# Optimization experiments

Hardware: AMD Instinct MI355X
Metric: run time of the kernel (lower is better)

The kernel has to match this reference:

```python
import jax, jax.numpy as jnp
import numpy as np

B, NPATCH, PDIM, DIM, OUTD = 4, 1024, 768, 512, 512
DIN, DSTATE, DTRANK, KCONV, NBLK = 2 * DIM, 16, DIM // 16, 4, 2


def _ln(x, w, b, eps=1e-5):
    m = jnp.mean(x, -1, keepdims=True)
    v = jnp.var(x, -1, keepdims=True)
    return (x - m) * jax.lax.rsqrt(v + eps) * w + b


def _mamba_block(x, ln_w, ln_b, in_W, conv_w, conv_b, xproj_W, dt_W, dt_b, A_log, Dp, out_W):
    # x: [b, L, dim]
    b, L, _ = x.shape
    xn = _ln(x, ln_w, ln_b)
    xz = xn @ in_W                                # [b, L, 2*DIN]
    u, z = jnp.split(xz, 2, axis=-1)              # each [b, L, DIN]
    # causal depthwise conv over time
    uc = jnp.transpose(u, (0, 2, 1))              # [b, DIN, L]
    uc = jax.lax.conv_general_dilated(
        uc, conv_w[:, None, :], window_strides=(1,), padding=((KCONV - 1, 0),),
        feature_group_count=DIN)
    uc = uc + conv_b[None, :, None]
    u = jax.nn.silu(jnp.transpose(uc, (0, 2, 1)))  # [b, L, DIN]
    x_dbl = u @ xproj_W                            # [b, L, DTRANK+2*DSTATE]
    dt, Bm, Cm = jnp.split(x_dbl, [DTRANK, DTRANK + DSTATE], axis=-1)
    delta = jax.nn.softplus(dt @ dt_W + dt_b)      # [b, L, DIN]
    A = -jnp.exp(A_log)                            # [DIN, DSTATE]
    dA = jnp.exp(delta[..., None] * A)             # [b, L, DIN, DSTATE]
    dBu = delta[..., None] * Bm[:, :, None, :] * u[..., None]  # [b, L, DIN, DSTATE]
    # selective scan over time
    def step(h, inp):
        dA_t, dBu_t, C_t = inp                     # [b,DIN,DSTATE],[b,DIN,DSTATE],[b,DSTATE]
        h = dA_t * h + dBu_t
        y = jnp.einsum('bdn,bn->bd', h, C_t)
        return h, y
    h0 = jnp.zeros((b, DIN, DSTATE), x.dtype)
    _, ys = jax.lax.scan(step, h0, (jnp.swapaxes(dA, 0, 1), jnp.swapaxes(dBu, 0, 1), jnp.swapaxes(Cm, 0, 1)))
    y = jnp.swapaxes(ys, 0, 1) + u * Dp            # [b, L, DIN]
    y = y * jax.nn.silu(z)
    return x + y @ out_W                           # residual


def setup_inputs() -> dict:
    key = jax.random.key(0)
    ks = iter(jax.random.split(key, 40))
    rn = lambda shape, s=0.02: jax.random.normal(next(ks), shape, jnp.float32) * s
    d = {
        'img': jax.random.normal(next(ks), (B, NPATCH, PDIM), jnp.float32),
        'patch_W': rn((PDIM, DIM)), 'patch_b': jnp.zeros((DIM,), jnp.float32),
        'pos_emb': rn((1, NPATCH + 1, DIM), 1.0), 'cls_tok': rn((1, 1, DIM), 1.0),
        'blk_ln_w': jnp.ones((NBLK, DIM)), 'blk_ln_b': jnp.zeros((NBLK, DIM)),
        'blk_in_W': rn((NBLK, DIM, 2 * DIN)),
        'blk_conv_w': rn((NBLK, DIN, KCONV), 0.1), 'blk_conv_b': jnp.zeros((NBLK, DIN)),
        'blk_xproj_W': rn((NBLK, DIN, DTRANK + 2 * DSTATE)),
        'blk_dt_W': rn((NBLK, DTRANK, DIN), 0.1), 'blk_dt_b': jnp.full((NBLK, DIN), -4.0),
        'blk_A_log': jnp.tile(jnp.log(jnp.arange(1, DSTATE + 1, dtype=jnp.float32))[None, None, :], (NBLK, DIN, 1)),
        'blk_D': jnp.ones((NBLK, DIN)),
        'blk_out_W': rn((NBLK, DIN, DIM)),
        'sl1_W': rn((DIM, OUTD)), 'sl1_b': jnp.zeros((OUTD,)),
        'sl1_lnw': jnp.ones((OUTD,)), 'sl1_lnb': jnp.zeros((OUTD,)),
        'sl2_W': rn((OUTD, OUTD)), 'sl2_b': jnp.zeros((OUTD,)),
        'sl2_lnw': jnp.ones((OUTD,)), 'sl2_lnb': jnp.zeros((OUTD,)),
        'lat_lnw': jnp.ones((OUTD,)), 'lat_lnb': jnp.zeros((OUTD,)),
    }
    return d


def reference(img, patch_W, patch_b, pos_emb, cls_tok,
              blk_ln_w, blk_ln_b, blk_in_W, blk_conv_w, blk_conv_b,
              blk_xproj_W, blk_dt_W, blk_dt_b, blk_A_log, blk_D, blk_out_W,
              sl1_W, sl1_b, sl1_lnw, sl1_lnb, sl2_W, sl2_b, sl2_lnw, sl2_lnb,
              lat_lnw, lat_lnb):
    x = img @ patch_W + patch_b                       # [b, n, dim]
    b, n, _ = x.shape
    cls = jnp.broadcast_to(cls_tok, (b, 1, DIM))
    x = jnp.concatenate([cls, x], axis=1) + pos_emb[:, :n + 1]
    for i in range(NBLK):
        x = _mamba_block(x, blk_ln_w[i], blk_ln_b[i], blk_in_W[i], blk_conv_w[i],
                         blk_conv_b[i], blk_xproj_W[i], blk_dt_W[i], blk_dt_b[i],
                         blk_A_log[i], blk_D[i], blk_out_W[i])
    y = jax.nn.gelu(_ln(x @ sl1_W + sl1_b, sl1_lnw, sl1_lnb), approximate=False)
    a = jax.nn.gelu(_ln(y @ sl2_W + sl2_b, sl2_lnw, sl2_lnb), approximate=False)
    z = jax.nn.softmax(a, axis=1)                     # softmax over sequence dim
    pooled = jnp.sum(y * z, axis=1)                   # [b, outdim]
    return _ln(pooled, lat_lnw, lat_lnb)
```

## Files before the change

### kernel.cpp

```cpp
#include <hip/hip_runtime.h>
#include <cstdint>
#include <cstddef>

#define B_     4
#define NPATCH 1024
#define LSEQ   1025
#define PDIM   768
#define DIM    512
#define OUTD   512
#define DIN    1024
#define DSTATE 16
#define DTRANK 32
#define KCONV  4
#define NBLK   2
#define MROWS  (B_*LSEQ)
#define NSEG_SP 17

typedef unsigned short u16;
typedef __attribute__((ext_vector_type(8))) short bf16x8;
typedef __attribute__((ext_vector_type(4))) float f32x4;

__device__ __forceinline__ float sigmoidf_(float x){ return 1.f/(1.f+__expf(-x)); }
__device__ __forceinline__ float geluf_(float x){ return 0.5f*x*(1.f+erff(x*0.70710678118654752f)); }
__device__ __forceinline__ u16 f2bf(float x){
    uint32_t b = __float_as_uint(x);
    b += 0x7FFFu + ((b >> 16) & 1u);
    return (u16)(b >> 16);
}
__device__ __forceinline__ float bf2f(u16 v){ return __uint_as_float((uint32_t)v << 16); }
template<int CTRL>
__device__ __forceinline__ float dppmov(float x){
    return __int_as_float(__builtin_amdgcn_update_dpp(0, __float_as_int(x), CTRL, 0xF, 0xF, true));
}
__device__ __forceinline__ float red16(float p){
    p += dppmov<0xB1>(p);
    p += dppmov<0x4E>(p);
    p += dppmov<0x141>(p);
    p += dppmov<0x140>(p);
    return p;
}
__device__ __forceinline__ void gload16(const void* g, void* l){
    __builtin_amdgcn_global_load_lds((const __attribute__((address_space(1))) void*)g,
                                     (__attribute__((address_space(3))) void*)l, 16, 0, 0);
}
__device__ __forceinline__ float softplusf_(float v){
    return (v > 20.f) ? v : log1pf(__expf(v));
}

template<int MF>
__global__ __launch_bounds__(256) void gemm_mfma(
    const u16* __restrict__ A, int lda,
    const u16* __restrict__ Wt,
    float* __restrict__ C, int ldc,
    int M, int N, int K,
    const float* __restrict__ bias,
    const float* __restrict__ addsrc,
    int act, u16* __restrict__ bf16out)
{
    __shared__ u16 lsA[MF*32*32];
    __shared__ u16 lsB[128*32];
    const int tid = threadIdx.x;
    const int wid = tid >> 6, lane = tid & 63;
    const int m0 = blockIdx.y * (MF*32), n0 = blockIdx.x * 128;
    const int wm = (wid>>1)*(MF*16), wn = (wid&1)*64;
    f32x4 acc[MF][4] = {};

    const char* Agp = (const char*)(A + (size_t)m0 * lda);
    const char* Bgp = (const char*)(Wt + (size_t)n0 * K);
    const int lrow = lane >> 2;
    const int lcb  = (((lane & 3) ^ ((lane >> 3) & 3))) * 16;
    const int rsw  = ((lane & 15) >> 1) & 3;
    const int acol = ((lane >> 4) ^ rsw) * 8;

    for (int k0 = 0; k0 < K; k0 += 32) {
        {
            int ra = wid*(MF*8) + lrow;
            gload16(Agp + (size_t)ra*(lda*2) + k0*2 + lcb, &lsA[(wid*(MF*8))*32]);
            if constexpr (MF == 4) {
                gload16(Agp + (size_t)(ra+16)*(lda*2) + k0*2 + lcb, &lsA[(wid*(MF*8)+16)*32]);
            }
        }
        {
            int rb = wid*32 + lrow;
            gload16(Bgp + (size_t)rb*(K*2) + k0*2 + lcb, &lsB[(wid*32)*32]);
            gload16(Bgp + (size_t)(rb+16)*(K*2) + k0*2 + lcb, &lsB[(wid*32+16)*32]);
        }
        __syncthreads();
        bf16x8 af[MF], bfr[4];
        #pragma unroll
        for (int i = 0; i < MF; ++i)
            af[i] = *(const bf16x8*)&lsA[(wm + i*16 + (lane&15))*32 + acol];
        #pragma unroll
        for (int j = 0; j < 4; ++j)
            bfr[j] = *(const bf16x8*)&lsB[(wn + j*16 + (lane&15))*32 + acol];
        #pragma unroll
        for (int i = 0; i < MF; ++i)
            #pragma unroll
            for (int j = 0; j < 4; ++j)
                acc[i][j] = __builtin_amdgcn_mfma_f32_16x16x32_bf16(af[i], bfr[j], acc[i][j], 0, 0, 0);
        __syncthreads();
    }
    #pragma unroll
    for (int i = 0; i < MF; ++i) {
        #pragma unroll
        for (int j = 0; j < 4; ++j) {
            int col = n0 + wn + j*16 + (lane & 15);
            float bv = bias ? bias[col] : 0.f;
            #pragma unroll
            for (int r = 0; r < 4; ++r) {
                int row = m0 + wm + i*16 + (lane>>4)*4 + r;
                if (row < M) {
                    float v = acc[i][j][r] + bv;
                    if (addsrc) v += addsrc[(size_t)row*ldc + col];
                    if (act == 1) v = softplusf_(v);
                    if (C) C[(size_t)row*ldc + col] = v;
                    if (bf16out) bf16out[(size_t)row*ldc + col] = f2bf(v);
                }
            }
        }
    }
}

__global__ __launch_bounds__(256) void xproj_gemm(
    const float* __restrict__ Au,
    const float* __restrict__ W,
    float* __restrict__ P)
{
    __shared__ float As[16][68];
    __shared__ float Bs[16][68];
    int tid = threadIdx.x;
    int tx = tid & 15, ty = tid >> 4;
    int m0 = blockIdx.x * 64;
    int kbase = blockIdx.y * 256;
    float acc[4][4] = {};
    for (int k0 = kbase; k0 < kbase + 256; k0 += 16) {
        {
            int r  = tid >> 2;
            int kq = (tid & 3) << 2;
            float4 va = make_float4(0.f,0.f,0.f,0.f);
            int gr = m0 + r;
            if (gr < MROWS) va = *reinterpret_cast<const float4*>(Au + (size_t)gr*DIN + k0 + kq);
            As[kq+0][r]=va.x; As[kq+1][r]=va.y; As[kq+2][r]=va.z; As[kq+3][r]=va.w;
        }
        {
            int kk = tid >> 4;
            int nq = (tid & 15) << 2;
            float4 vb = *reinterpret_cast<const float4*>(W + (size_t)(k0+kk)*64 + nq);
            Bs[kk][nq+0]=vb.x; Bs[kk][nq+1]=vb.y; Bs[kk][nq+2]=vb.z; Bs[kk][nq+3]=vb.w;
        }
        __syncthreads();
        #pragma unroll
        for (int k = 0; k < 16; ++k) {
            float a0=As[k][ty*4+0],a1=As[k][ty*4+1],a2=As[k][ty*4+2],a3=As[k][ty*4+3];
            float b0=Bs[k][tx*4+0],b1=Bs[k][tx*4+1],b2=Bs[k][tx*4+2],b3=Bs[k][tx*4+3];
            acc[0][0]=fmaf(a0,b0,acc[0][0]); acc[0][1]=fmaf(a0,b1,acc[0][1]);
            acc[0][2]=fmaf(a0,b2,acc[0][2]); acc[0][3]=fmaf(a0,b3,acc[0][3]);
            acc[1][0]=fmaf(a1,b0,acc[1][0]); acc[1][1]=fmaf(a1,b1,acc[1][1]);
            acc[1][2]=fmaf(a1,b2,acc[1][2]); acc[1][3]=fmaf(a1,b3,acc[1][3]);
            acc[2][0]=fmaf(a2,b0,acc[2][0]); acc[2][1]=fmaf(a2,b1,acc[2][1]);
            acc[2][2]=fmaf(a2,b2,acc[2][2]); acc[2][3]=fmaf(a2,b3,acc[2][3]);
            acc[3][0]=fmaf(a3,b0,acc[3][0]); acc[3][1]=fmaf(a3,b1,acc[3][1]);
            acc[3][2]=fmaf(a3,b2,acc[3][2]); acc[3][3]=fmaf(a3,b3,acc[3][3]);
        }
        __syncthreads();
    }
    float* Pp = P + (size_t)blockIdx.y * (MROWS*64);
    #pragma unroll
    for (int i = 0; i < 4; ++i) {
        int r = m0 + ty*4 + i;
        if (r >= MROWS) continue;
        #pragma unroll
        for (int j = 0; j < 4; ++j)
            Pp[(size_t)r*64 + tx*4 + j] = acc[i][j];
    }
}

__global__ __launch_bounds__(256) void xproj_reduce(
    const float* __restrict__ P, float* __restrict__ xdbl)
{
    int idx = blockIdx.x*256 + threadIdx.x;
    xdbl[idx] = P[idx] + P[MROWS*64 + idx] + P[2*MROWS*64 + idx] + P[3*MROWS*64 + idx];
}

__device__ void tcast(const float* __restrict__ in, u16* __restrict__ outp,
                      int K, int N, int tix)
{
    __shared__ float tl[32][33];
    int ntn = N >> 5;
    int tk = tix / ntn, tn = tix - tk*ntn;
    int tid = threadIdx.x;
    int r = tid >> 3, c0 = (tid & 7) << 2;
    float4 v = *(const float4*)&in[(size_t)(tk*32 + r)*N + tn*32 + c0];
    tl[r][c0+0]=v.x; tl[r][c0+1]=v.y; tl[r][c0+2]=v.z; tl[r][c0+3]=v.w;
    __syncthreads();
    int nn = r, k0 = c0;
    uint32_t w0 = f2bf(tl[k0+0][nn]) | ((uint32_t)f2bf(tl[k0+1][nn]) << 16);
    uint32_t w1 = f2bf(tl[k0+2][nn]) | ((uint32_t)f2bf(tl[k0+3][nn]) << 16);
    uint2 o; o.x = w0; o.y = w1;
    *(uint2*)&outp[(size_t)(tn*32 + nn)*K + tk*32 + k0] = o;
}

__global__ __launch_bounds__(256) void prep_kernel(
    const float* __restrict__ img, const float* __restrict__ pW,
    const float* __restrict__ inW, const float* __restrict__ outW,
    const float* __restrict__ s1W, const float* __restrict__ s2W,
    u16* imgb, u16* pWt, u16* inWt, u16* outWt, u16* s1t, u16* s2t)
{
    int b = blockIdx.x;
    if (b < 3072) {
        int idx = b*1024 + threadIdx.x*4;
        float4 v = *(const float4*)&img[idx];
        uint2 o;
        o.x = f2bf(v.x) | ((uint32_t)f2bf(v.y) << 16);
        o.y = f2bf(v.z) | ((uint32_t)f2bf(v.w) << 16);
        *(uint2*)&imgb[idx] = o;
        return;
    }
    b -= 3072;
    if (b < 384)  { tcast(pW, pWt, 768, 512, b); return; }
    b -= 384;
    if (b < 2048) { int blk=b>>10, t=b&1023; tcast(inW + (size_t)blk*512*2048, inWt + (size_t)blk*1048576, 512, 2048, t); return; }
    b -= 2048;
    if (b < 1024) { int blk=b>>9, t=b&511; tcast(outW + (size_t)blk*1024*512, outWt + (size_t)blk*524288, 1024, 512, t); return; }
    b -= 1024;
    if (b < 256)  { tcast(s1W, s1t, 512, 512, b); return; }
    b -= 256;
    tcast(s2W, s2t, 512, 512, b);
}

__global__ __launch_bounds__(256) void assemble_x(
    const float* __restrict__ tmp, const float* __restrict__ cls,
    const float* __restrict__ pos, float* __restrict__ x)
{
    int idx = blockIdx.x*256 + threadIdx.x;
    int d = idx & 511;
    int r = idx >> 9;
    int l = r % LSEQ;
    int b = r / LSEQ;
    float v = (l == 0) ? cls[d] : tmp[((size_t)(b*NPATCH + l-1))*DIM + d];
    x[idx] = v + pos[(size_t)l*DIM + d];
}

__global__ __launch_bounds__(256) void ln_act(
    const float* __restrict__ in, const float* __restrict__ gw, const float* __restrict__ gb,
    float* __restrict__ f32out, u16* __restrict__ bf16out, int act)
{
    int row = blockIdx.x;
    const float* p = in + (size_t)row * 512;
    int t = threadIdx.x;
    float v0 = p[t], v1 = p[t + 256];
    float s = v0 + v1, q = v0*v0 + v1*v1;
    #pragma unroll
    for (int o = 32; o; o >>= 1) { s += __shfl_xor(s, o); q += __shfl_xor(q, o); }
    __shared__ float ls[4], lq[4];
    int w = t >> 6;
    if ((t & 63) == 0) { ls[w] = s; lq[w] = q; }
    __syncthreads();
    s = ls[0]+ls[1]+ls[2]+ls[3];
    q = lq[0]+lq[1]+lq[2]+lq[3];
    float mean = s * (1.f/512.f);
    float var  = q * (1.f/512.f) - mean*mean;
    float inv  = rsqrtf(var + 1e-5f);
    float o0 = (v0-mean)*inv*gw[t]     + gb[t];
    float o1 = (v1-mean)*inv*gw[t+256] + gb[t+256];
    if (act == 2) { o0 = geluf_(o0); o1 = geluf_(o1); }
    if (f32out)  { f32out[(size_t)row*512 + t] = o0; f32out[(size_t)row*512 + t + 256] = o1; }
    if (bf16out) { bf16out[(size_t)row*512 + t] = f2bf(o0); bf16out[(size_t)row*512 + t + 256] = f2bf(o1); }
}

__global__ __launch_bounds__(256) void conv_silu(
    const u16* __restrict__ xzb, const float* __restrict__ cw,
    const float* __restrict__ cb, float* __restrict__ uo)
{
    int idx = blockIdx.x*256 + threadIdx.x;
    int dq = idx & 255;
    int r  = idx >> 8;
    int b = r / LSEQ, l = r - b*LSEQ;
    int d0 = dq << 2;
    float4 w0 = *(const float4*)&cw[(d0+0)*4];
    float4 w1 = *(const float4*)&cw[(d0+1)*4];
    float4 w2 = *(const float4*)&cw[(d0+2)*4];
    float4 w3 = *(const float4*)&cw[(d0+3)*4];
    float4 acc = *(const float4*)&cb[d0];
    const float* wv0 = &w0.x; const float* wv1 = &w1.x;
    const float* wv2 = &w2.x; const float* wv3 = &w3.x;
    #pragma unroll
    for (int k = 0; k < KCONV; ++k) {
        int ls = l - (KCONV-1) + k;
        if (ls >= 0) {
            ushort4 v = *(const ushort4*)&xzb[((size_t)(b*LSEQ + ls))*2048 + d0];
            acc.x = fmaf(wv0[k], bf2f(v.x), acc.x);
            acc.y = fmaf(wv1[k], bf2f(v.y), acc.y);
            acc.z = fmaf(wv2[k], bf2f(v.z), acc.z);
            acc.w = fmaf(wv3[k], bf2f(v.w), acc.w);
        }
    }
    acc.x *= sigmoidf_(acc.x);
    acc.y *= sigmoidf_(acc.y);
    acc.z *= sigmoidf_(acc.z);
    acc.w *= sigmoidf_(acc.w);
    *(float4*)&uo[(size_t)r*DIN + d0] = acc;
}

__global__ __launch_bounds__(256) void scan_phase1(
    const float* __restrict__ u,    const float* __restrict__ xdbl,
    const float* __restrict__ dtW,  const float* __restrict__ dtb,
    const float* __restrict__ A_log,
    float* __restrict__ Aseg, float* __restrict__ Hseg)
{
    const int dg = blockIdx.x, b = blockIdx.y, s = blockIdx.z;
    const int tid = threadIdx.x;
    const int n = tid & 15, dl = tid >> 4;
    const int tr = tid >> 4, tc = tid & 15;
    const int d0 = dg*16, d = d0 + dl;
    const float Adn2 = -__expf(A_log[(size_t)d*DSTATE + n]) * 1.44269504f;
    __shared__ float sX[16][68];
    __shared__ float sW[32][17];
    __shared__ float sU[16][20];
    __shared__ float sDel[16][20];
    {
        int k = tid >> 4;
        sW[k][tc]    = dtW[(size_t)k*DIN + d0 + tc];
        sW[k+16][tc] = dtW[(size_t)(k+16)*DIN + d0 + tc];
    }
    const float db = dtb[d0 + tc];
    float sdv = 0.f, h = 0.f;
    const size_t base = (size_t)b*LSEQ + (size_t)s*128;
    for (int c0 = 0; c0 < 128; c0 += 16) {
        __syncthreads();
        {
            size_t row = base + c0 + tr;
            *(float4*)&sX[tr][tc*4] = *(const float4*)&xdbl[row*64 + tc*4];
            sU[tc][tr] = u[row*DIN + d0 + tc];
        }
        __syncthreads();
        {
            float acc = db;
            #pragma unroll
            for (int k = 0; k < 32; ++k) acc = fmaf(sX[tr][k], sW[k][tc], acc);
            sDel[tc][tr] = softplusf_(acc);
        }
        __syncthreads();
        #pragma unroll
        for (int hf = 0; hf < 2; ++hf) {
            f32x4 vD0 = *(const f32x4*)&sDel[dl][hf*8];
            f32x4 vD1 = *(const f32x4*)&sDel[dl][hf*8+4];
            f32x4 vU0 = *(const f32x4*)&sU[dl][hf*8];
            f32x4 vU1 = *(const f32x4*)&sU[dl][hf*8+4];
            #pragma unroll
            for (int t = 0; t < 8; ++t) {
                float dv = (t<4) ? vD0[t&3] : vD1[t&3];
                float uv = (t<4) ? vU0[t&3] : vU1[t&3];
                float Bv = sX[hf*8+t][32+n];
                sdv += dv;
                h = fmaf(__builtin_exp2f(dv * Adn2), h, dv*uv*Bv);
            }
        }
    }
    int dn = d*DSTATE + n;
    Aseg[((size_t)b*7 + s)*16384 + dn] = __builtin_exp2f(Adn2 * sdv);
    Hseg[((size_t)b*8 + s)*16384 + dn] = h;
}

__global__ __launch_bounds__(256) void scan_mid(
    float* __restrict__ Hseg, const float* __restrict__ Aseg)
{
    int idx = blockIdx.x*256 + threadIdx.x;
    int b = idx >> 14, dn = idx & 16383;
    float prev = 0.f;
    #pragma unroll
    for (int s = 0; s < 7; ++s) {
        size_t offH = ((size_t)b*8 + s)*16384 + dn;
        float a  = Aseg[((size_t)b*7 + s)*16384 + dn];
        float hs = Hseg[offH];
        Hseg[offH] = prev;
        prev = fmaf(a, prev, hs);
    }
    Hseg[((size_t)b*8 + 7)*16384 + dn] = prev;
}

__global__ __launch_bounds__(256) void scan_phase2(
    const float* __restrict__ u,    const float* __restrict__ xdbl,
    const u16*   __restrict__ xzb,  const float* __restrict__ dtW,
    const float* __restrict__ dtb,  const float* __restrict__ A_log,
    const float* __restrict__ Dp,   const float* __restrict__ H0,
    u16* __restrict__ yb)
{
    const int dg = blockIdx.x, b = blockIdx.y, s = blockIdx.z;
    const int tid = threadIdx.x;
    const int n = tid & 15, dl = tid >> 4;
    const int tr = tid >> 4, tc = tid & 15;
    const int d0 = dg*16, d = d0 + dl;
    const float Adn2 = -__expf(A_log[(size_t)d*DSTATE + n]) * 1.44269504f;
    const float Dd = Dp[d];
    float h = H0[((size_t)b*8 + s)*16384 + d*DSTATE + n];
    __shared__ float sX[16][68];
    __shared__ float sW[32][17];
    __shared__ float sU[16][20];
    __shared__ float sDel[16][20];
    __shared__ float sZ[16][20];
    __shared__ u16 sY[16][17];
    {
        int k = tid >> 4;
        sW[k][tc]    = dtW[(size_t)k*DIN + d0 + tc];
        sW[k+16][tc] = dtW[(size_t)(k+16)*DIN + d0 + tc];
    }
    const float db = dtb[d0 + tc];
    const size_t base = (size_t)b*LSEQ + (size_t)s*128;
    for (int c0 = 0; c0 < 128; c0 += 16) {
        {
            size_t row = base + c0 + tr;
            *(float4*)&sX[tr][tc*4] = *(const float4*)&xdbl[row*64 + tc*4];
            sU[tc][tr] = u[row*DIN + d0 + tc];
            sZ[tc][tr] = bf2f(xzb[row*2048 + DIN + d0 + tc]);
        }
        __syncthreads();
        {
            float acc = db;
            #pragma unroll
            for (int k = 0; k < 32; ++k) acc = fmaf(sX[tr][k], sW[k][tc], acc);
            sDel[tc][tr] = softplusf_(acc);
        }
        __syncthreads();
        float py = 0.f;
        #pragma unroll
        for (int hf = 0; hf < 2; ++hf) {
            f32x4 vD0 = *(const f32x4*)&sDel[dl][hf*8];
            f32x4 vD1 = *(const f32x4*)&sDel[dl][hf*8+4];
            f32x4 vU0 = *(const f32x4*)&sU[dl][hf*8];
            f32x4 vU1 = *(const f32x4*)&sU[dl][hf*8+4];
            #pragma unroll
            for (int t = 0; t < 8; ++t) {
                float dv = (t<4) ? vD0[t&3] : vD1[t&3];
                float uv = (t<4) ? vU0[t&3] : vU1[t&3];
                int tt = hf*8 + t;
                float Bv = sX[tt][32+n];
                float Cv = sX[tt][48+n];
                h = fmaf(__builtin_exp2f(dv * Adn2), h, dv*uv*Bv);
                float pr = red16(h * Cv);
                py = (n == tt) ? pr : py;
            }
        }
        {
            float uv = sU[dl][n];
            float zv = sZ[dl][n];
            sY[n][dl] = f2bf((py + uv*Dd) * (zv * sigmoidf_(zv)));
        }
        __syncthreads();
        yb[(base + c0 + tr)*DIN + d0 + tc] = sY[tr][tc];
    }
    if (s == 7) {
        size_t row = (size_t)b*LSEQ + 1024;
        float acc = dtb[d];
        #pragma unroll
        for (int k = 0; k < 32; ++k)
            acc = fmaf(xdbl[row*64 + k], dtW[(size_t)k*DIN + d], acc);
        float dv = softplusf_(acc);
        float uv = u[row*DIN + d];
        float zv = bf2f(xzb[row*2048 + DIN + d]);
        float Bv = xdbl[row*64 + DTRANK + n];
        float Cv = xdbl[row*64 + DTRANK + DSTATE + n];
        h = fmaf(__builtin_exp2f(dv * Adn2), h, dv*uv*Bv);
        float p = red16(h * Cv);
        if (n == 0)
            yb[row*DIN + d] = f2bf((p + uv*Dd) * (zv * sigmoidf_(zv)));
    }
}

__global__ __launch_bounds__(256) void softpool_seg(
    const float* __restrict__ a, const float* __restrict__ yh,
    float* __restrict__ pm, float* __restrict__ ps, float* __restrict__ pp)
{
    int b   = blockIdx.y;
    int seg = blockIdx.z;
    int jj = threadIdx.x & 63;
    int j  = blockIdx.x * 64 + jj;
    int li = threadIdx.x >> 6;
    int lbeg = seg * 64;
    int lend = min(lbeg + 64, LSEQ);
    float m = -3.0e38f, s = 0.f, p = 0.f;
    for (int l = lbeg + li; l < lend; l += 4) {
        size_t off = ((size_t)(b*LSEQ + l))*OUTD + j;
        float av = a[off], yv = yh[off];
        float mn = fmaxf(m, av);
        float sc = __expf(m - mn);
        float e  = __expf(av - mn);
        s = s*sc + e;
        p = p*sc + yv*e;
        m = mn;
    }
    __shared__ float sm[4][64], ss[4][64], sp[4][64];
    sm[li][jj] = m; ss[li][jj] = s; sp[li][jj] = p;
    __syncthreads();
    if (li == 0) {
        #pragma unroll
        for (int k2 = 1; k2 < 4; ++k2) {
            float m2 = sm[k2][jj], s2 = ss[k2][jj], p2 = sp[k2][jj];
            float M2 = fmaxf(m, m2);
            float c1 = __expf(m - M2), c2 = __expf(m2 - M2);
            s = s*c1 + s2*c2;
            p = p*c1 + p2*c2;
            m = M2;
        }
        int o = ((seg*B_ + b)*OUTD) + j;
        pm[o] = m; ps[o] = s; pp[o] = p;
    }
}

__global__ __launch_bounds__(256) void softpool_combine(
    const float* __restrict__ pm, const float* __restrict__ ps,
    const float* __restrict__ pp, float* __restrict__ pooled)
{
    int idx = blockIdx.x*256 + threadIdx.x;
    int b = idx >> 9, j = idx & 511;
    float m = -3.0e38f, s = 0.f, p = 0.f;
    #pragma unroll
    for (int seg = 0; seg < NSEG_SP; ++seg) {
        int o = ((seg*B_ + b)*OUTD) + j;
        float m2 = pm[o], s2 = ps[o], p2 = pp[o];
        float M2 = fmaxf(m, m2);
        float c1 = __expf(m - M2), c2 = __expf(m2 - M2);
        s = s*c1 + s2*c2;
        p = p*c1 + p2*c2;
        m = M2;
    }
    pooled[(size_t)b*OUTD + j] = p / s;
}

extern "C" void kernel_launch(void* const* d_in, const int* in_sizes, int n_in,
                              void* d_out, int out_size, void* d_ws, size_t ws_size,
                              hipStream_t stream) {
    const float* img     = (const float*)d_in[0];
    const float* patch_W = (const float*)d_in[1];
    const float* patch_b = (const float*)d_in[2];
    const float* pos_emb = (const float*)d_in[3];
    const float* cls_tok = (const float*)d_in[4];
    const float* ln_w    = (const float*)d_in[5];
    const float* ln_b    = (const float*)d_in[6];
    const float* in_W    = (const float*)d_in[7];
    const float* conv_w  = (const float*)d_in[8];
    const float* conv_b  = (const float*)d_in[9];
    const float* xproj_W = (const float*)d_in[10];
    const float* dt_W    = (const float*)d_in[11];
    const float* dt_b    = (const float*)d_in[12];
    const float* A_log   = (const float*)d_in[13];
    const float* Dp      = (const float*)d_in[14];
    const float* out_W   = (const float*)d_in[15];
    const float* sl1_W   = (const float*)d_in[16];
    const float* sl1_b   = (const float*)d_in[17];
    const float* sl1_lnw = (const float*)d_in[18];
    const float* sl1_lnb = (const float*)d_in[19];
    const float* sl2_W   = (const float*)d_in[20];
    const float* sl2_b   = (const float*)d_in[21];
    const float* sl2_lnw = (const float*)d_in[22];
    const float* sl2_lnb = (const float*)d_in[23];
    const float* lat_lnw = (const float*)d_in[24];
    const float* lat_lnb = (const float*)d_in[25];
    float* out = (float*)d_out;
    float* ws  = (float*)d_ws;

    float* x      = ws + 0;
    u16*   xz_bf  = (u16*)(ws + 2099200);
    float* yh     = ws + 6297600;
    float* t2     = ws + 8396800;
    float* u      = ws + 10496000;
    float* xdbl   = ws + 14694400;
    float* scratch= ws + 14956800;
    u16* ub      = (u16*)(ws + 19155200);
    u16* regA    = ub + 0;
    u16* regB    = ub + 4325376;
    u16* pWt     = ub + 6758400;
    u16* inWt    = ub + 7151616;
    u16* outWt   = ub + 9248768;
    u16* s1t     = ub + 10362880;
    u16* s2t     = ub + 10625024;

    float* a      = u;
    float* pooled = xdbl;
    float* spm    = xdbl + 8192;
    float* sps    = spm + 34816;
    float* spp    = sps + 34816;
    float* t1     = scratch;
    float* xprojP = scratch;
    float* segH   = (float*)regB;
    float* segA   = segH + 524288;

    prep_kernel<<<7040, 256, 0, stream>>>(img, patch_W, in_W, out_W, sl1_W, sl2_W,
                                          regA, pWt, inWt, outWt, s1t, s2t);

    gemm_mfma<2><<<dim3(512/128, 4096/64), 256, 0, stream>>>(
        regA, PDIM, pWt, scratch, DIM, 4096, DIM, PDIM, patch_b, nullptr, 0, nullptr);
    assemble_x<<<(MROWS*DIM)/256, 256, 0, stream>>>(scratch, cls_tok, pos_emb, x);

    for (int i = 0; i < NBLK; ++i) {
        ln_act<<<MROWS, 256, 0, stream>>>(x, ln_w + i*DIM, ln_b + i*DIM,
                                          nullptr, regB, 0);
        gemm_mfma<4><<<dim3(2048/128, 33), 256, 0, stream>>>(
            regB, DIM, inWt + (size_t)i*1048576, nullptr, 2048,
            MROWS, 2*DIN, DIM, nullptr, nullptr, 0, xz_bf);
        conv_silu<<<MROWS, 256, 0, stream>>>(
            xz_bf, conv_w + i*DIN*KCONV, conv_b + i*DIN, u);
        xproj_gemm<<<dim3(65, 4), 256, 0, stream>>>(
            u, xproj_W + (size_t)i*DIN*64, xprojP);
        xproj_reduce<<<1025, 256, 0, stream>>>(xprojP, xdbl);
        scan_phase1<<<dim3(64, 4, 7), 256, 0, stream>>>(
            u, xdbl, dt_W + (size_t)i*DTRANK*DIN, dt_b + i*DIN,
            A_log + (size_t)i*DIN*DSTATE, segA, segH);
        scan_mid<<<256, 256, 0, stream>>>(segH, segA);
        scan_phase2<<<dim3(64, 4, 8), 256, 0, stream>>>(
            u, xdbl, xz_bf, dt_W + (size_t)i*DTRANK*DIN, dt_b + i*DIN,
            A_log + (size_t)i*DIN*DSTATE, Dp + i*DIN, segH, regA);
        gemm_mfma<2><<<dim3(512/128, 65), 256, 0, stream>>>(
            regA, DIN, outWt + (size_t)i*524288, x, DIM,
            MROWS, DIM, DIN, nullptr, x, 0, (i == NBLK-1) ? regB : nullptr);
    }

    gemm_mfma<2><<<dim3(512/128, 65), 256, 0, stream>>>(
        regB, DIM, s1t, t1, OUTD, MROWS, OUTD, DIM, sl1_b, nullptr, 0, nullptr);
    ln_act<<<MROWS, 256, 0, stream>>>(t1, sl1_lnw, sl1_lnb, yh, regA, 2);
    gemm_mfma<2><<<dim3(512/128, 65), 256, 0, stream>>>(
        regA, OUTD, s2t, t2, OUTD, MROWS, OUTD, OUTD, sl2_b, nullptr, 0, nullptr);
    ln_act<<<MROWS, 256, 0, stream>>>(t2, sl2_lnw, sl2_lnb, a, nullptr, 2);
    softpool_seg<<<dim3(OUTD/64, B_, NSEG_SP), 256, 0, stream>>>(a, yh, spm, sps, spp);
    softpool_combine<<<8, 256, 0, stream>>>(spm, sps, spp, pooled);
    ln_act<<<B_, 256, 0, stream>>>(pooled, lat_lnw, lat_lnb, out, nullptr, 0);
}
```

Baseline: 610.1 us.

## Replace three-pass chunked selective scan with single sequential pipelined scan kernel

Merges the segment scan, carry propagation and output pass into one kernel where each block scans its whole sequence for 16 channels. Inputs are prefetched into registers and double-buffered in shared memory in 64-step chunks, and dt weights are kept in registers. This removes the extra pass over u and xdbl and two kernel launches, but cuts the grid to 256 blocks and lengthens each block's serial dependency chain, which reduces parallelism.

After: 635.5 us. 1.04x slower.

```diff
diff --git a/kernel.cpp b/kernel.cpp
--- a/kernel.cpp
+++ b/kernel.cpp
@@ -302,155 +302,107 @@
     *(float4*)&uo[(size_t)r*DIN + d0] = acc;
 }
 
-__global__ __launch_bounds__(256) void scan_phase1(
-    const float* __restrict__ u,    const float* __restrict__ xdbl,
-    const float* __restrict__ dtW,  const float* __restrict__ dtb,
-    const float* __restrict__ A_log,
-    float* __restrict__ Aseg, float* __restrict__ Hseg)
-{
-    const int dg = blockIdx.x, b = blockIdx.y, s = blockIdx.z;
-    const int tid = threadIdx.x;
-    const int n = tid & 15, dl = tid >> 4;
-    const int tr = tid >> 4, tc = tid & 15;
-    const int d0 = dg*16, d = d0 + dl;
-    const float Adn2 = -__expf(A_log[(size_t)d*DSTATE + n]) * 1.44269504f;
-    __shared__ float sX[16][68];
-    __shared__ float sW[32][17];
-    __shared__ float sU[16][20];
-    __shared__ float sDel[16][20];
-    {
-        int k = tid >> 4;
-        sW[k][tc]    = dtW[(size_t)k*DIN + d0 + tc];
-        sW[k+16][tc] = dtW[(size_t)(k+16)*DIN + d0 + tc];
-    }
-    const float db = dtb[d0 + tc];
-    float sdv = 0.f, h = 0.f;
-    const size_t base = (size_t)b*LSEQ + (size_t)s*128;
-    for (int c0 = 0; c0 < 128; c0 += 16) {
-        __syncthreads();
-        {
-            size_t row = base + c0 + tr;
-            *(float4*)&sX[tr][tc*4] = *(const float4*)&xdbl[row*64 + tc*4];
-            sU[tc][tr] = u[row*DIN + d0 + tc];
-        }
-        __syncthreads();
-        {
-            float acc = db;
-            #pragma unroll
-            for (int k = 0; k < 32; ++k) acc = fmaf(sX[tr][k], sW[k][tc], acc);
-            sDel[tc][tr] = softplusf_(acc);
-        }
-        __syncthreads();
-        #pragma unroll
-        for (int hf = 0; hf < 2; ++hf) {
-            f32x4 vD0 = *(const f32x4*)&sDel[dl][hf*8];
-            f32x4 vD1 = *(const f32x4*)&sDel[dl][hf*8+4];
-            f32x4 vU0 = *(const f32x4*)&sU[dl][hf*8];
-            f32x4 vU1 = *(const f32x4*)&sU[dl][hf*8+4];
-            #pragma unroll
-            for (int t = 0; t < 8; ++t) {
-                float dv = (t<4) ? vD0[t&3] : vD1[t&3];
-                float uv = (t<4) ? vU0[t&3] : vU1[t&3];
-                float Bv = sX[hf*8+t][32+n];
-                sdv += dv;
-                h = fmaf(__builtin_exp2f(dv * Adn2), h, dv*uv*Bv);
-            }
-        }
-    }
-    int dn = d*DSTATE + n;
-    Aseg[((size_t)b*7 + s)*16384 + dn] = __builtin_exp2f(Adn2 * sdv);
-    Hseg[((size_t)b*8 + s)*16384 + dn] = h;
-}
-
-__global__ __launch_bounds__(256) void scan_mid(
-    float* __restrict__ Hseg, const float* __restrict__ Aseg)
-{
-    int idx = blockIdx.x*256 + threadIdx.x;
-    int b = idx >> 14, dn = idx & 16383;
-    float prev = 0.f;
-    #pragma unroll
-    for (int s = 0; s < 7; ++s) {
-        size_t offH = ((size_t)b*8 + s)*16384 + dn;
-        float a  = Aseg[((size_t)b*7 + s)*16384 + dn];
-        float hs = Hseg[offH];
-        Hseg[offH] = prev;
-        prev = fmaf(a, prev, hs);
-    }
-    Hseg[((size_t)b*8 + 7)*16384 + dn] = prev;
-}
-
-__global__ __launch_bounds__(256) void scan_phase2(
+__global__ __launch_bounds__(256) void scan_full(
     const float* __restrict__ u,    const float* __restrict__ xdbl,
     const u16*   __restrict__ xzb,  const float* __restrict__ dtW,
     const float* __restrict__ dtb,  const float* __restrict__ A_log,
-    const float* __restrict__ Dp,   const float* __restrict__ H0,
-    u16* __restrict__ yb)
-{
-    const int dg = blockIdx.x, b = blockIdx.y, s = blockIdx.z;
+    const float* __restrict__ Dp,   u16* __restrict__ yb)
+{
+    const int dg = blockIdx.x, b = blockIdx.y;
     const int tid = threadIdx.x;
     const int n = tid & 15, dl = tid >> 4;
-    const int tr = tid >> 4, tc = tid & 15;
     const int d0 = dg*16, d = d0 + dl;
     const float Adn2 = -__expf(A_log[(size_t)d*DSTATE + n]) * 1.44269504f;
     const float Dd = Dp[d];
-    float h = H0[((size_t)b*8 + s)*16384 + d*DSTATE + n];
-    __shared__ float sX[16][68];
-    __shared__ float sW[32][17];
-    __shared__ float sU[16][20];
-    __shared__ float sDel[16][20];
-    __shared__ float sZ[16][20];
-    __shared__ u16 sY[16][17];
-    {
-        int k = tid >> 4;
-        sW[k][tc]    = dtW[(size_t)k*DIN + d0 + tc];
-        sW[k+16][tc] = dtW[(size_t)(k+16)*DIN + d0 + tc];
-    }
-    const float db = dtb[d0 + tc];
-    const size_t base = (size_t)b*LSEQ + (size_t)s*128;
-    for (int c0 = 0; c0 < 128; c0 += 16) {
-        {
-            size_t row = base + c0 + tr;
-            *(float4*)&sX[tr][tc*4] = *(const float4*)&xdbl[row*64 + tc*4];
-            sU[tc][tr] = u[row*DIN + d0 + tc];
-            sZ[tc][tr] = bf2f(xzb[row*2048 + DIN + d0 + tc]);
-        }
-        __syncthreads();
-        {
+
+    __shared__ float sX[2][64][68];
+    __shared__ float sU[2][16][68];
+    __shared__ float sZ[2][16][68];
+    __shared__ float sDel[16][68];
+    __shared__ u16  sY[64][17];
+
+    float rW[32];
+    #pragma unroll
+    for (int k = 0; k < 32; ++k) rW[k] = dtW[(size_t)k*DIN + d0 + n];
+    const float db = dtb[d0 + n];
+
+    const size_t base = (size_t)b * LSEQ;
+    const int sr = tid >> 2;
+    const int sq = tid & 3;
+
+    float4 rX[4]; float4 rU; ushort4 rZ;
+    auto LOADG = [&](int c){
+        size_t row = base + (size_t)c*64 + sr;
+        #pragma unroll
+        for (int j = 0; j < 4; ++j)
+            rX[j] = *(const float4*)&xdbl[row*64 + sq*16 + j*4];
+        rU = *(const float4*)&u[row*DIN + d0 + sq*4];
+        rZ = *(const ushort4*)&xzb[row*2048 + DIN + d0 + sq*4];
+    };
+    auto WRITES = [&](int pb){
+        #pragma unroll
+        for (int j = 0; j < 4; ++j)
+            *(float4*)&sX[pb][sr][sq*16 + j*4] = rX[j];
+        sU[pb][sq*4+0][sr] = rU.x; sU[pb][sq*4+1][sr] = rU.y;
+        sU[pb][sq*4+2][sr] = rU.z; sU[pb][sq*4+3][sr] = rU.w;
+        sZ[pb][sq*4+0][sr] = bf2f(rZ.x); sZ[pb][sq*4+1][sr] = bf2f(rZ.y);
+        sZ[pb][sq*4+2][sr] = bf2f(rZ.z); sZ[pb][sq*4+3][sr] = bf2f(rZ.w);
+    };
+
+    LOADG(0); WRITES(0);
+    __syncthreads();
+    float h = 0.f;
+    for (int c = 0; c < 16; ++c) {
+        const int pb = c & 1;
+        if (c < 15) LOADG(c+1);
+        #pragma unroll
+        for (int sub = 0; sub < 4; ++sub) {
+            int t = sub*16 + dl;
             float acc = db;
             #pragma unroll
-            for (int k = 0; k < 32; ++k) acc = fmaf(sX[tr][k], sW[k][tc], acc);
-            sDel[tc][tr] = softplusf_(acc);
-        }
-        __syncthreads();
-        float py = 0.f;
-        #pragma unroll
-        for (int hf = 0; hf < 2; ++hf) {
-            f32x4 vD0 = *(const f32x4*)&sDel[dl][hf*8];
-            f32x4 vD1 = *(const f32x4*)&sDel[dl][hf*8+4];
-            f32x4 vU0 = *(const f32x4*)&sU[dl][hf*8];
-            f32x4 vU1 = *(const f32x4*)&sU[dl][hf*8+4];
+            for (int k = 0; k < 32; ++k) acc = fmaf(sX[pb][t][k], rW[k], acc);
+            sDel[n][t] = softplusf_(acc);
+        }
+        __syncthreads();
+        #pragma unroll
+        for (int sub = 0; sub < 4; ++sub) {
+            float Bv[16], Cv[16];
             #pragma unroll
-            for (int t = 0; t < 8; ++t) {
-                float dv = (t<4) ? vD0[t&3] : vD1[t&3];
-                float uv = (t<4) ? vU0[t&3] : vU1[t&3];
-                int tt = hf*8 + t;
-                float Bv = sX[tt][32+n];
-                float Cv = sX[tt][48+n];
-                h = fmaf(__builtin_exp2f(dv * Adn2), h, dv*uv*Bv);
-                float pr = red16(h * Cv);
-                py = (n == tt) ? pr : py;
+            for (int t = 0; t < 16; ++t) {
+                Bv[t] = sX[pb][sub*16+t][DTRANK + n];
+                Cv[t] = sX[pb][sub*16+t][DTRANK + DSTATE + n];
             }
-        }
+            f32x4 vD[4], vU[4];
+            #pragma unroll
+            for (int q4 = 0; q4 < 4; ++q4) {
+                vD[q4] = *(const f32x4*)&sDel[dl][sub*16 + q4*4];
+                vU[q4] = *(const f32x4*)&sU[pb][dl][sub*16 + q4*4];
+            }
+            float py = 0.f;
+            #pragma unroll
+            for (int t = 0; t < 16; ++t) {
+                float dv = vD[t>>2][t&3];
+                float uv = vU[t>>2][t&3];
+                h = fmaf(__builtin_exp2f(dv * Adn2), h, dv*uv*Bv[t]);
+                float pr = red16(h * Cv[t]);
+                py = (n == t) ? pr : py;
+            }
+            float uv_e = sU[pb][dl][sub*16 + n];
+            float zv   = sZ[pb][dl][sub*16 + n];
+            sY[sub*16 + n][dl] = f2bf((py + uv_e*Dd) * (zv * sigmoidf_(zv)));
+        }
+        __syncthreads();
         {
-            float uv = sU[dl][n];
-            float zv = sZ[dl][n];
-            sY[n][dl] = f2bf((py + uv*Dd) * (zv * sigmoidf_(zv)));
-        }
-        __syncthreads();
-        yb[(base + c0 + tr)*DIN + d0 + tc] = sY[tr][tc];
-    }
-    if (s == 7) {
-        size_t row = (size_t)b*LSEQ + 1024;
+            ushort4 o;
+            o.x = sY[sr][sq*4+0]; o.y = sY[sr][sq*4+1];
+            o.z = sY[sr][sq*4+2]; o.w = sY[sr][sq*4+3];
+            *(ushort4*)&yb[(base + (size_t)c*64 + sr)*DIN + d0 + sq*4] = o;
+        }
+        if (c < 15) WRITES((c+1) & 1);
+        __syncthreads();
+    }
+    {
+        size_t row = base + 1024;
         float acc = dtb[d];
         #pragma unroll
         for (int k = 0; k < 32; ++k)
@@ -582,8 +534,6 @@
     float* spp    = sps + 34816;
     float* t1     = scratch;
     float* xprojP = scratch;
-    float* segH   = (float*)regB;
-    float* segA   = segH + 524288;
 
     prep_kernel<<<7040, 256, 0, stream>>>(img, patch_W, in_W, out_W, sl1_W, sl2_W,
                                           regA, pWt, inWt, outWt, s1t, s2t);
@@ -603,13 +553,9 @@
         xproj_gemm<<<dim3(65, 4), 256, 0, stream>>>(
             u, xproj_W + (size_t)i*DIN*64, xprojP);
         xproj_reduce<<<1025, 256, 0, stream>>>(xprojP, xdbl);
-        scan_phase1<<<dim3(64, 4, 7), 256, 0, stream>>>(
-            u, xdbl, dt_W + (size_t)i*DTRANK*DIN, dt_b + i*DIN,
-            A_log + (size_t)i*DIN*DSTATE, segA, segH);
-        scan_mid<<<256, 256, 0, stream>>>(segH, segA);
-        scan_phase2<<<dim3(64, 4, 8), 256, 0, stream>>>(
+        scan_full<<<dim3(64, 4), 256, 0, stream>>>(
             u, xdbl, xz_bf, dt_W + (size_t)i*DTRANK*DIN, dt_b + i*DIN,
-            A_log + (size_t)i*DIN*DSTATE, Dp + i*DIN, segH, regA);
+            A_log + (size_t)i*DIN*DSTATE, Dp + i*DIN, regA);
         gemm_mfma<2><<<dim3(512/128, 65), 256, 0, stream>>>(
             regA, DIN, outWt + (size_t)i*524288, x, DIM,
             MROWS, DIM, DIN, nullptr, x, 0, (i == NBLK-1) ? regB : nullptr);
```

## Double-buffer GEMM LDS tiles and split selective scan into more segments

Applied to the files above, without the earlier changes.

The MFMA GEMM now uses two LDS buffers, so the next K-tile's global-to-LDS loads are issued while the current tile is being consumed. This is meant to overlap memory latency with the matrix math, at the cost of twice the shared memory per block. The chunked selective scan goes from 8 segments of 128 steps to 16 segments of 64 steps. That halves the serial recurrence length per block and doubles the number of blocks, in exchange for a longer sequential combine in scan_mid. The segment state buffers move into the scratch region to fit the larger size, and an extra barrier is added in scan_phase2's chunk loop.

Measured after the change: 636.5 us. 4.3% more time.

```diff
diff --git a/kernel.cpp b/kernel.cpp
--- a/kernel.cpp
+++ b/kernel.cpp
@@ -15,6 +15,8 @@
 #define NBLK   2
 #define MROWS  (B_*LSEQ)
 #define NSEG_SP 17
+#define SEGLEN 64
+#define NSEGS  16
 
 typedef unsigned short u16;
 typedef __attribute__((ext_vector_type(8))) short bf16x8;
@@ -57,8 +59,8 @@
     const float* __restrict__ addsrc,
     int act, u16* __restrict__ bf16out)
 {
-    __shared__ u16 lsA[MF*32*32];
-    __shared__ u16 lsB[128*32];
+    __shared__ u16 lsA[2][MF*32*32];
+    __shared__ u16 lsB[2][128*32];
     const int tid = threadIdx.x;
     const int wid = tid >> 6, lane = tid & 63;
     const int m0 = blockIdx.y * (MF*32), n0 = blockIdx.x * 128;
@@ -72,27 +74,29 @@
     const int rsw  = ((lane & 15) >> 1) & 3;
     const int acol = ((lane >> 4) ^ rsw) * 8;
 
-    for (int k0 = 0; k0 < K; k0 += 32) {
-        {
-            int ra = wid*(MF*8) + lrow;
-            gload16(Agp + (size_t)ra*(lda*2) + k0*2 + lcb, &lsA[(wid*(MF*8))*32]);
-            if constexpr (MF == 4) {
-                gload16(Agp + (size_t)(ra+16)*(lda*2) + k0*2 + lcb, &lsA[(wid*(MF*8)+16)*32]);
-            }
-        }
-        {
-            int rb = wid*32 + lrow;
-            gload16(Bgp + (size_t)rb*(K*2) + k0*2 + lcb, &lsB[(wid*32)*32]);
-            gload16(Bgp + (size_t)(rb+16)*(K*2) + k0*2 + lcb, &lsB[(wid*32+16)*32]);
-        }
-        __syncthreads();
+    const int nt = K >> 5;
+    auto STAGE = [&](int buf, int k0){
+        int ra = wid*(MF*8) + lrow;
+        gload16(Agp + (size_t)ra*(lda*2) + k0*2 + lcb, &lsA[buf][(wid*(MF*8))*32]);
+        if constexpr (MF == 4)
+            gload16(Agp + (size_t)(ra+16)*(lda*2) + k0*2 + lcb, &lsA[buf][(wid*(MF*8)+16)*32]);
+        int rb = wid*32 + lrow;
+        gload16(Bgp + (size_t)rb*(K*2) + k0*2 + lcb, &lsB[buf][(wid*32)*32]);
+        gload16(Bgp + (size_t)(rb+16)*(K*2) + k0*2 + lcb, &lsB[buf][(wid*32+16)*32]);
+    };
+
+    STAGE(0, 0);
+    __syncthreads();
+    for (int kt = 0; kt < nt; ++kt) {
+        const int cur = kt & 1;
+        if (kt + 1 < nt) STAGE(cur ^ 1, (kt+1) * 32);
         bf16x8 af[MF], bfr[4];
         #pragma unroll
         for (int i = 0; i < MF; ++i)
-            af[i] = *(const bf16x8*)&lsA[(wm + i*16 + (lane&15))*32 + acol];
+            af[i] = *(const bf16x8*)&lsA[cur][(wm + i*16 + (lane&15))*32 + acol];
         #pragma unroll
         for (int j = 0; j < 4; ++j)
-            bfr[j] = *(const bf16x8*)&lsB[(wn + j*16 + (lane&15))*32 + acol];
+            bfr[j] = *(const bf16x8*)&lsB[cur][(wn + j*16 + (lane&15))*32 + acol];
         #pragma unroll
         for (int i = 0; i < MF; ++i)
             #pragma unroll
@@ -325,8 +329,8 @@
     }
     const float db = dtb[d0 + tc];
     float sdv = 0.f, h = 0.f;
-    const size_t base = (size_t)b*LSEQ + (size_t)s*128;
-    for (int c0 = 0; c0 < 128; c0 += 16) {
+    const size_t base = (size_t)b*LSEQ + (size_t)s*SEGLEN;
+    for (int c0 = 0; c0 < SEGLEN; c0 += 16) {
         __syncthreads();
         {
             size_t row = base + c0 + tr;
@@ -351,15 +355,15 @@
             for (int t = 0; t < 8; ++t) {
                 float dv = (t<4) ? vD0[t&3] : vD1[t&3];
                 float uv = (t<4) ? vU0[t&3] : vU1[t&3];
-                float Bv = sX[hf*8+t][32+n];
+                float Bv = sX[hf*8+t][DTRANK+n];
                 sdv += dv;
                 h = fmaf(__builtin_exp2f(dv * Adn2), h, dv*uv*Bv);
             }
         }
     }
     int dn = d*DSTATE + n;
-    Aseg[((size_t)b*7 + s)*16384 + dn] = __builtin_exp2f(Adn2 * sdv);
-    Hseg[((size_t)b*8 + s)*16384 + dn] = h;
+    Aseg[((size_t)b*(NSEGS-1) + s)*16384 + dn] = __builtin_exp2f(Adn2 * sdv);
+    Hseg[((size_t)b*NSEGS + s)*16384 + dn] = h;
 }
 
 __global__ __launch_bounds__(256) void scan_mid(
@@ -369,14 +373,14 @@
     int b = idx >> 14, dn = idx & 16383;
     float prev = 0.f;
     #pragma unroll
-    for (int s = 0; s < 7; ++s) {
-        size_t offH = ((size_t)b*8 + s)*16384 + dn;
-        float a  = Aseg[((size_t)b*7 + s)*16384 + dn];
+    for (int s = 0; s < NSEGS-1; ++s) {
+        size_t offH = ((size_t)b*NSEGS + s)*16384 + dn;
+        float a  = Aseg[((size_t)b*(NSEGS-1) + s)*16384 + dn];
         float hs = Hseg[offH];
         Hseg[offH] = prev;
         prev = fmaf(a, prev, hs);
     }
-    Hseg[((size_t)b*8 + 7)*16384 + dn] = prev;
+    Hseg[((size_t)b*NSEGS + NSEGS-1)*16384 + dn] = prev;
 }
 
 __global__ __launch_bounds__(256) void scan_phase2(
@@ -393,7 +397,7 @@
     const int d0 = dg*16, d = d0 + dl;
     const float Adn2 = -__expf(A_log[(size_t)d*DSTATE + n]) * 1.44269504f;
     const float Dd = Dp[d];
-    float h = H0[((size_t)b*8 + s)*16384 + d*DSTATE + n];
+    float h = H0[((size_t)b*NSEGS + s)*16384 + d*DSTATE + n];
     __shared__ float sX[16][68];
     __shared__ float sW[32][17];
     __shared__ float sU[16][20];
@@ -406,8 +410,8 @@
         sW[k+16][tc] = dtW[(size_t)(k+16)*DIN + d0 + tc];
     }
     const float db = dtb[d0 + tc];
-    const size_t base = (size_t)b*LSEQ + (size_t)s*128;
-    for (int c0 = 0; c0 < 128; c0 += 16) {
+    const size_t base = (size_t)b*LSEQ + (size_t)s*SEGLEN;
+    for (int c0 = 0; c0 < SEGLEN; c0 += 16) {
         {
             size_t row = base + c0 + tr;
             *(float4*)&sX[tr][tc*4] = *(const float4*)&xdbl[row*64 + tc*4];
@@ -434,8 +438,8 @@
                 float dv = (t<4) ? vD0[t&3] : vD1[t&3];
                 float uv = (t<4) ? vU0[t&3] : vU1[t&3];
                 int tt = hf*8 + t;
-                float Bv = sX[tt][32+n];
-                float Cv = sX[tt][48+n];
+                float Bv = sX[tt][DTRANK+n];
+                float Cv = sX[tt][DTRANK+DSTATE+n];
                 h = fmaf(__builtin_exp2f(dv * Adn2), h, dv*uv*Bv);
                 float pr = red16(h * Cv);
                 py = (n == tt) ? pr : py;
@@ -448,8 +452,9 @@
         }
         __syncthreads();
         yb[(base + c0 + tr)*DIN + d0 + tc] = sY[tr][tc];
-    }
-    if (s == 7) {
+        __syncthreads();
+    }
+    if (s == NSEGS-1) {
         size_t row = (size_t)b*LSEQ + 1024;
         float acc = dtb[d];
         #pragma unroll
@@ -582,8 +587,8 @@
     float* spp    = sps + 34816;
     float* t1     = scratch;
     float* xprojP = scratch;
-    float* segH   = (float*)regB;
-    float* segA   = segH + 524288;
+    float* segH   = scratch;
+    float* segA   = scratch + 1048576;
 
     prep_kernel<<<7040, 256, 0, stream>>>(img, patch_W, in_W, out_W, sl1_W, sl2_W,
                                           regA, pWt, inWt, outWt, s1t, s2t);
@@ -603,11 +608,11 @@
         xproj_gemm<<<dim3(65, 4), 256, 0, stream>>>(
             u, xproj_W + (size_t)i*DIN*64, xprojP);
         xproj_reduce<<<1025, 256, 0, stream>>>(xprojP, xdbl);
-        scan_phase1<<<dim3(64, 4, 7), 256, 0, stream>>>(
+        scan_phase1<<<dim3(64, 4, NSEGS-1), 256, 0, stream>>>(
             u, xdbl, dt_W + (size_t)i*DTRANK*DIN, dt_b + i*DIN,
             A_log + (size_t)i*DIN*DSTATE, segA, segH);
         scan_mid<<<256, 256, 0, stream>>>(segH, segA);
-        scan_phase2<<<dim3(64, 4, 8), 256, 0, stream>>>(
+        scan_phase2<<<dim3(64, 4, NSEGS), 256, 0, stream>>>(
             u, xdbl, xz_bf, dt_W + (size_t)i*DTRANK*DIN, dt_b + i*DIN,
             A_log + (size_t)i*DIN*DSTATE, Dp + i*DIN, segH, regA);
         gemm_mfma<2><<<dim3(512/128, 65), 256, 0, stream>>>(
```
